# Kernel optimization log

Hardware: AMD Instinct MI355X
Metric: run time of the kernel (lower is better)

The kernel has to match this reference:

```python
import jax, jax.numpy as jnp
from jax import lax
import numpy as np

# HH / synapse constants (CFG in original repo; standard values matching the rate eqns)
GNA, GK, GL = 40.0, 35.0, 0.3
ENA, EK, EL = 55.0, -77.0, -65.0
GS, VS = 1.0, 0.0
IAPP = 1.0
VT, KP = -20.0, 3.0
A_D, A_R = 1.0, 0.1
DT = 0.02

B, N, L = 16, 2000, 1024


def setup_inputs() -> dict:
    key = jax.random.key(0)
    z = jax.random.uniform(key, (B, N, L), dtype=jnp.float32)
    return {"z": z}


def _rates(V):
    # Singularity-safe rate constants (the torch code patches V==25 / V==-35 exactly).
    at25 = V == 25.0
    atm35 = V == -35.0
    dN = jnp.where(at25, 1.0, 1.0 - jnp.exp((-V + 25.0) / 9.0))
    dM = jnp.where(atm35, 1.0, 1.0 - jnp.exp((-V - 35.0) / 9.0))
    dNb = jnp.where(at25, 1.0, 1.0 - jnp.exp((V - 25.0) / 9.0))
    dMb = jnp.where(atm35, 1.0, 1.0 - jnp.exp((V + 35.0) / 9.0))
    aN = jnp.where(at25, 0.18, 0.02 * (V - 25.0) / dN)
    bN = jnp.where(at25, 0.08, -0.002 * (V - 25.0) / dNb)
    aM = jnp.where(atm35, 1.638, 0.182 * (V + 35.0) / dM)
    bM = jnp.where(atm35, 1.16, -0.124 * (V + 35.0) / dMb)
    aH = 0.25 * jnp.exp((-V - 90.0) / 12.0)
    bH = 0.25 * jnp.exp((V + 34.0) / 12.0)
    return aN, bN, aM, bM, aH, bH


def _step(carry, z_prev):
    V, m, n, h, y = carry
    pow1 = GNA * m ** 3 * h
    pow2 = GK * n ** 4
    G = DT / 2 * (pow1 + pow2 + GL + GS * y)
    E = pow1 * ENA + pow2 * EK + GL * EL + GS * VS * y
    Vn = (V * (1.0 - G) + DT * (E + IAPP)) / (1.0 + G)
    aN, bN, aM, bM, aH, bH = _rates(Vn)
    mn = (aM * DT + (1.0 - DT / 2 * (aM + bM)) * m) / (DT / 2 * (aM + bM) + 1.0)
    nn = (aN * DT + (1.0 - DT / 2 * (aN + bN)) * n) / (DT / 2 * (aN + bN) + 1.0)
    hn = (aH * DT + (1.0 - DT / 2 * (aH + bH)) * h) / (DT / 2 * (aH + bH) + 1.0)
    ady = A_D * z_prev
    yn = (ady * DT + (1.0 - DT / 2 * (ady + A_R)) * y) / (DT / 2 * (ady + A_R) + 1.0)
    return (Vn, mn, nn, hn, yn), Vn


def _hh(z):
    b, n_t, l = z.shape
    zt = jnp.moveaxis(z, 1, 0)  # (N, B, L); step k uses z[k-1]
    V0 = jnp.full((b, l), -70.0, dtype=z.dtype)
    zeros = jnp.zeros((b, l), dtype=z.dtype)
    ones = jnp.ones((b, l), dtype=z.dtype)
    carry0 = (V0, zeros, zeros, ones, zeros)
    _, Vseq = lax.scan(_step, carry0, zt[:-1])  # (N-1, B, L)
    Vall = jnp.concatenate([V0[None], Vseq], axis=0)  # (N, B, L)
    V = jnp.moveaxis(Vall, 0, 1)  # (B, N, L)
    return jax.nn.sigmoid((V - VT) / KP)


def reference(z):
    return _hh(z)
```

## Files before the change

### kernel.cpp

```cpp
#include <hip/hip_runtime.h>

#define N_ 2000
#define L_ 1024

__device__ __forceinline__ float rcpf(float d) { return __builtin_amdgcn_rcpf(d); }
__device__ __forceinline__ float ex2(float x)  { return __builtin_amdgcn_exp2f(x); }

#define STEP1(K, RS)                                                          \
  {                                                                           \
    const int kk = (K);                                                       \
    float zc = zb[RS];                                                        \
    int kpre = kk + 7;                                                        \
    int kc = kpre < 1998 ? kpre : 1998;                                       \
    zb[RS] = z[base + kc * L_];                                               \
     \
    float m2   = m * m;                                                       \
    float m3   = m2 * m;                                                      \
    float valm = m3 * h;                                           \
    float n2   = n * n;                                                       \
    float valn = n2 * n2;                                            \
    float gy   = __fmaf_rn(y, 0.01f, 0.003f);                                 \
    float G    = __fmaf_rn(valm, 0.4f, __fmaf_rn(valn, 0.35f, gy));           \
    float E    = __fmaf_rn(valm, 2200.0f, __fmaf_rn(valn, -2695.0f, -19.5f)); \
    float num  = __fmaf_rn(V, 1.0f - G, __fmaf_rn(E, 0.02f, 0.02f));          \
    float Vn   = num * rcpf(1.0f + G);                                        \
        \
    float eRm  = ex2(__fmaf_rn(Vn, K9, 35.0f * K9));                          \
    float um   = Vn + 35.0f;                                                  \
    float urm  = um * rcpf(eRm - 1.0f);                                       \
    bool  patm = (Vn == -35.0f);                                              \
    float aM   = patm ? 1.638f   : 0.182f * (urm * eRm);                      \
    float s1m  = patm ? 0.02798f : urm * __fmaf_rn(0.00182f, eRm, 0.00124f);  \
                                           \
    float eRn  = ex2(__fmaf_rn(Vn, K9, -25.0f * K9));                         \
    float un   = Vn - 25.0f;                                                  \
    float urn  = un * rcpf(eRn - 1.0f);                                       \
    bool  patn = (Vn == 25.0f);                                               \
    float aN   = patn ? 0.18f   : 0.02f * (urn * eRn);                        \
    float s1n  = patn ? 0.0026f : urn * __fmaf_rn(0.0002f, eRn, 0.00002f);    \
                                                                 \
    float aH   = 0.25f * ex2(__fmaf_rn(Vn, -K12, -90.0f * K12));              \
    float bH   = 0.25f * ex2(__fmaf_rn(Vn,  K12,  34.0f * K12));              \
                                                \
    float qm   = 1.0f + s1m;                                                  \
    float numm = __fmaf_rn(aM, 0.02f, __fmaf_rn(-s1m, m, m));                 \
    float qn   = 1.0f + s1n;                                                  \
    float numn = __fmaf_rn(aN, 0.02f, __fmaf_rn(-s1n, n, n));                 \
    float sh   = __fmaf_rn(aH, 0.01f, 0.01f * bH);                            \
    float qh   = 1.0f + sh;                                                   \
    float numh = __fmaf_rn(aH, 0.02f, __fmaf_rn(-sh, h, h));                  \
    float sy   = __fmaf_rn(zc, 0.01f, 0.001f);                                \
    float qy   = 1.0f + sy;                                                   \
    float numy = __fmaf_rn(zc, 0.02f, __fmaf_rn(-sy, y, y));                  \
    float rq1  = rcpf(qm * qh);                                               \
    m = numm * (rq1 * qh);                                                    \
    h = numh * (rq1 * qm);                                                    \
    float rq2  = rcpf(qn * qy);                                               \
    n = numn * (rq2 * qy);                                                    \
    y = numy * (rq2 * qn);                                                    \
    V = Vn;                                                                   \
                          \
    float e2 = eRm * eRm;                                                     \
    float ts = (e2 * eRm) * 0.006737946999085467f;                            \
    float sg = ts * rcpf(1.0f + ts);                                          \
    out[base + kk * L_] = sg;                                                 \
  }

__global__ __launch_bounds__(64) void hh_kernel(const float* __restrict__ z,
                                                float* __restrict__ out) {
    const int t   = blockIdx.x * 64 + threadIdx.x;
    const int b   = t >> 10;
    const int l   = t & 1023;
    const int base = b * (N_ * L_) + l;

    const float K9  = 0.16029944898766259f;
    const float K12 = 0.12022458674074695f;

    float V = -70.0f;
    float m = 0.0f, n = 0.0f, h = 1.0f, y = 0.0f;

    float zb[8];
#pragma unroll
    for (int i = 0; i < 8; ++i) zb[i] = z[base + i * L_];

    out[base] = 5.777750e-8f;

    int k = 1;
    for (int g = 0; g < 249; ++g) {
#pragma unroll
        for (int j = 0; j < 8; ++j) {
            STEP1(k + j, j)
        }
        k += 8;
    }
#pragma unroll
    for (int j = 0; j < 7; ++j) {
        STEP1(k + j, j)
    }
}

extern "C" void kernel_launch(void* const* d_in, const int* in_sizes, int n_in,
                              void* d_out, int out_size, void* d_ws, size_t ws_size,
                              hipStream_t stream) {
    const float* z = (const float*)d_in[0];
    float* out = (float*)d_out;
    hh_kernel<<<256, 64, 0, stream>>>(z, out);
}
```

Before: 510.2 us.

## Deepen z prefetch, shorten V update dependency chain, regroup reciprocals, nontemporal stores

```diff
diff --git a/kernel.cpp b/kernel.cpp
--- a/kernel.cpp
+++ b/kernel.cpp
@@ -10,60 +10,64 @@
   {                                                                           \
     const int kk = (K);                                                       \
     float zc = zb[RS];                                                        \
-    int kpre = kk + 7;                                                        \
+    int kpre = kk + 15;                                                       \
     int kc = kpre < 1998 ? kpre : 1998;                                       \
     zb[RS] = z[base + kc * L_];                                               \
-     \
+                            \
+    float mh   = m * h;                                                       \
     float m2   = m * m;                                                       \
-    float m3   = m2 * m;                                                      \
-    float valm = m3 * h;                                           \
+    float valm = m2 * mh;                                          \
     float n2   = n * n;                                                       \
-    float valn = n2 * n2;                                            \
+    float valn = n2 * n2;                                           \
     float gy   = __fmaf_rn(y, 0.01f, 0.003f);                                 \
     float G    = __fmaf_rn(valm, 0.4f, __fmaf_rn(valn, 0.35f, gy));           \
     float E    = __fmaf_rn(valm, 2200.0f, __fmaf_rn(valn, -2695.0f, -19.5f)); \
-    float num  = __fmaf_rn(V, 1.0f - G, __fmaf_rn(E, 0.02f, 0.02f));          \
-    float Vn   = num * rcpf(1.0f + G);                                        \
-        \
+            \
+    float r    = rcpf(1.0f + G);                                              \
+    float tVD  = __fmaf_rn(E, 0.02f, __fmaf_rn(2.0f, V, 0.02f));              \
+    float Vn   = __fmaf_rn(tVD, r, -V);                                       \
+                                                               \
     float eRm  = ex2(__fmaf_rn(Vn, K9, 35.0f * K9));                          \
+    float eRn  = ex2(__fmaf_rn(Vn, K9, -25.0f * K9));                         \
+    float rrm  = rcpf(eRm - 1.0f);                                            \
+    float rrn  = rcpf(eRn - 1.0f);                                            \
     float um   = Vn + 35.0f;                                                  \
-    float urm  = um * rcpf(eRm - 1.0f);                                       \
-    bool  patm = (Vn == -35.0f);                                              \
-    float aM   = patm ? 1.638f   : 0.182f * (urm * eRm);                      \
-    float s1m  = patm ? 0.02798f : urm * __fmaf_rn(0.00182f, eRm, 0.00124f);  \
-                                           \
-    float eRn  = ex2(__fmaf_rn(Vn, K9, -25.0f * K9));                         \
     float un   = Vn - 25.0f;                                                  \
-    float urn  = un * rcpf(eRn - 1.0f);                                       \
-    bool  patn = (Vn == 25.0f);                                               \
-    float aN   = patn ? 0.18f   : 0.02f * (urn * eRn);                        \
-    float s1n  = patn ? 0.0026f : urn * __fmaf_rn(0.0002f, eRn, 0.00002f);    \
-                                                                 \
+    float urm  = um * rrm;                                                    \
+    float urn  = un * rrn;                                                    \
+    float Xm   = __fmaf_rn(0.00182f, eRm, 0.00124f);                          \
+    float Xn   = __fmaf_rn(0.0002f,  eRn, 0.00002f);                          \
+    float sm   = urm * Xm;                                                    \
+    float sn   = urn * Xn;                                                    \
+    float aM   = 0.182f * (urm * eRm);                                        \
+    float aN   = 0.02f  * (urn * eRn);                                        \
+    bool patm  = (Vn == -35.0f);                                              \
+    bool patn  = (Vn == 25.0f);                                               \
+    sm = patm ? 0.02798f : sm;  aM = patm ? 1.638f : aM;                      \
+    sn = patn ? 0.0026f  : sn;  aN = patn ? 0.18f  : aN;                      \
+          \
+    float numm = __fmaf_rn(aM, 0.02f, __fmaf_rn(-sm, m, m));                  \
+    float numn = __fmaf_rn(aN, 0.02f, __fmaf_rn(-sn, n, n));                  \
+    m = numm * rcpf(1.0f + sm);                                               \
+    n = numn * rcpf(1.0f + sn);                                               \
+                              \
     float aH   = 0.25f * ex2(__fmaf_rn(Vn, -K12, -90.0f * K12));              \
     float bH   = 0.25f * ex2(__fmaf_rn(Vn,  K12,  34.0f * K12));              \
-                                                \
-    float qm   = 1.0f + s1m;                                                  \
-    float numm = __fmaf_rn(aM, 0.02f, __fmaf_rn(-s1m, m, m));                 \
-    float qn   = 1.0f + s1n;                                                  \
-    float numn = __fmaf_rn(aN, 0.02f, __fmaf_rn(-s1n, n, n));                 \
     float sh   = __fmaf_rn(aH, 0.01f, 0.01f * bH);                            \
+    float numh = __fmaf_rn(aH, 0.02f, __fmaf_rn(-sh, h, h));                  \
     float qh   = 1.0f + sh;                                                   \
-    float numh = __fmaf_rn(aH, 0.02f, __fmaf_rn(-sh, h, h));                  \
     float sy   = __fmaf_rn(zc, 0.01f, 0.001f);                                \
+    float numy = __fmaf_rn(zc, 0.02f, __fmaf_rn(-sy, y, y));                  \
     float qy   = 1.0f + sy;                                                   \
-    float numy = __fmaf_rn(zc, 0.02f, __fmaf_rn(-sy, y, y));                  \
-    float rq1  = rcpf(qm * qh);                                               \
-    m = numm * (rq1 * qh);                                                    \
-    h = numh * (rq1 * qm);                                                    \
-    float rq2  = rcpf(qn * qy);                                               \
-    n = numn * (rq2 * qy);                                                    \
-    y = numy * (rq2 * qn);                                                    \
+    float rq   = rcpf(qh * qy);                                               \
+    h = numh * (rq * qy);                                                     \
+    y = numy * (rq * qh);                                                     \
     V = Vn;                                                                   \
-                          \
+                     \
     float e2 = eRm * eRm;                                                     \
     float ts = (e2 * eRm) * 0.006737946999085467f;                            \
     float sg = ts * rcpf(1.0f + ts);                                          \
-    out[base + kk * L_] = sg;                                                 \
+    __builtin_nontemporal_store(sg, &out[base + kk * L_]);                    \
   }
 
 __global__ __launch_bounds__(64) void hh_kernel(const float* __restrict__ z,
@@ -79,22 +83,22 @@
     float V = -70.0f;
     float m = 0.0f, n = 0.0f, h = 1.0f, y = 0.0f;
 
-    float zb[8];
+    float zb[16];
 #pragma unroll
-    for (int i = 0; i < 8; ++i) zb[i] = z[base + i * L_];
+    for (int i = 0; i < 16; ++i) zb[i] = z[base + i * L_];
 
-    out[base] = 5.777750e-8f;
+    __builtin_nontemporal_store(5.777750e-8f, &out[base]);
 
     int k = 1;
-    for (int g = 0; g < 249; ++g) {
+    for (int g = 0; g < 124; ++g) {
 #pragma unroll
-        for (int j = 0; j < 8; ++j) {
+        for (int j = 0; j < 16; ++j) {
             STEP1(k + j, j)
         }
-        k += 8;
+        k += 16;
     }
 #pragma unroll
-    for (int j = 0; j < 7; ++j) {
+    for (int j = 0; j < 15; ++j) {
         STEP1(k + j, j)
     }
 }
```

Result: slower. 521.8 us (+2.3%).
